# Kernel tuning notes

Hardware: AMD Instinct MI355X
Metric: run time of the kernel (lower is better)

## Reference

```python
import jax, jax.numpy as jnp
import numpy as np
from jax import lax

ANCHORS = jnp.array([[-83.0, -39.0, 100.0, 56.0], [-175.0, -87.0, 192.0, 104.0],
                     [-359.0, -183.0, 376.0, 200.0], [-55.0, -55.0, 72.0, 72.0],
                     [-119.0, -119.0, 136.0, 136.0], [-247.0, -247.0, 264.0, 264.0],
                     [-35.0, -79.0, 52.0, 96.0], [-79.0, -167.0, 96.0, 184.0],
                     [-167.0, -343.0, 184.0, 360.0]], dtype=jnp.float32)
FEAT_STRIDE = 16
NMS_THRESH = 0.7
NA = 9
PRE_NMS_TOPN = 3000   # test_pre_nms_topN
POST_NMS_TOPN = 300   # test_post_nms_topN


def setup_inputs() -> dict:
    key = jax.random.key(0)
    ks = jax.random.split(key, 4)
    B, C, H, W = 8, 512, 64, 64
    x = jax.random.normal(ks[0], (B, C, H, W), jnp.float32)
    im_size = jnp.full((B, 2), 1024.0, jnp.float32)  # (H, W) per image
    W_conv = jax.random.normal(ks[1], (512, C, 3, 3), jnp.float32) * 0.01
    b_conv = jnp.zeros((512,), jnp.float32)
    W_reg = jax.random.normal(ks[2], (36, 512), jnp.float32) * 0.01
    b_reg = jnp.zeros((36,), jnp.float32)
    W_cls = jax.random.normal(ks[3], (18, 512), jnp.float32) * 0.01
    b_cls = jnp.zeros((18,), jnp.float32)
    return {"x": x, "im_size": im_size, "W_conv": W_conv, "b_conv": b_conv,
            "W_reg": W_reg, "b_reg": b_reg, "W_cls": W_cls, "b_cls": b_cls}


def _nms_select(boxes):
    """Greedy NMS on boxes already sorted by descending score.
    Returns [POST_NMS_TOPN, 4], zero-padded (matches torch output init)."""
    M = boxes.shape[0]
    area = (boxes[:, 2] - boxes[:, 0]) * (boxes[:, 3] - boxes[:, 1])
    lt = jnp.maximum(boxes[:, None, :2], boxes[None, :, :2])
    rb = jnp.minimum(boxes[:, None, 2:], boxes[None, :, 2:])
    wh = jnp.maximum(rb - lt, 0.0)
    inter = wh[..., 0] * wh[..., 1]
    iou = inter / (area[:, None] + area[None, :] - inter + 1e-9)
    iou = lax.stop_gradient(iou)
    idxs = jnp.arange(M)

    def body(keep, i):
        sup = (iou[i] > NMS_THRESH) & (idxs > i) & keep[i]
        return keep & ~sup, None

    keep, _ = lax.scan(body, jnp.ones((M,), bool), idxs)
    key = jnp.where(keep, idxs, M)           # push suppressed to the end
    order = jnp.sort(key)[:POST_NMS_TOPN]
    valid = order < M
    gi = jnp.minimum(order, M - 1)
    return jnp.where(valid[:, None], boxes[gi], 0.0)


def reference(x, im_size, W_conv, b_conv, W_reg, b_reg, W_cls, b_cls):
    B = x.shape[0]
    conv = lax.conv_general_dilated(
        x, W_conv, window_strides=(1, 1), padding='SAME',
        dimension_numbers=('NCHW', 'OIHW', 'NCHW')) + b_conv[None, :, None, None]
    Hc, Wc = conv.shape[2], conv.shape[3]

    # bbox deltas from raw (pre-ReLU) conv features, as in the source
    reg = jnp.einsum('bchw,oc->bohw', conv, W_reg) + b_reg[None, :, None, None]
    delta = reg.transpose(0, 2, 3, 1).reshape(B, -1, 4)  # (B, H*W*9, 4)

    # scores from ReLU'd features; channel-pair softmax trick, take class 0
    feat = jax.nn.relu(conv)
    cls = jnp.einsum('bchw,oc->bohw', feat, W_cls) + b_cls[None, :, None, None]
    c2 = cls.reshape(B, 2, NA * Hc, Wc)
    scores = jax.nn.softmax(c2, axis=1)[:, 0].reshape(B, -1)  # (B, 9*H*W)

    # anchor shifting: (h, w, anchor) ordering matches delta layout
    sx = jnp.arange(Wc, dtype=x.dtype) * FEAT_STRIDE
    sy = jnp.arange(Hc, dtype=x.dtype) * FEAT_STRIDE
    gx, gy = jnp.meshgrid(sx, sy)  # (Hc, Wc) 'xy' indexing
    shifts = jnp.stack([gx.ravel(), gy.ravel(), gx.ravel(), gy.ravel()], axis=1)
    anc = (shifts[:, None, :] + ANCHORS[None, :, :]).reshape(-1, 4)  # (H*W*9, 4)

    # decode, faithful to the source's (nonstandard) math
    w = anc[:, 2] - anc[:, 0] + 1.0
    h = anc[:, 3] - anc[:, 1] + 1.0
    cx = anc[:, 0] + 0.5 * w
    cy = anc[:, 1] + 0.5 * h
    dx, dy, dw, dh = delta[..., 0], delta[..., 1], delta[..., 2], delta[..., 3]
    pcx = dx * cx
    pcy = dy * cy
    pw = jnp.exp(dw) * w
    ph = jnp.exp(dh) * h
    x1, y1 = pcx - 0.5 * pw, pcy - 0.5 * ph
    x2, y2 = pcx + 0.5 * pw, pcy + 0.5 * ph

    # clip to image bounds (im_size[i] = (H, W))
    xmax = im_size[:, 1:2] - 1.0  # (B,1)
    ymax = im_size[:, 0:1] - 1.0
    x1 = jnp.clip(x1, 0.0, xmax)
    y1 = jnp.clip(y1, 0.0, ymax)
    x2 = jnp.clip(x2, 0.0, xmax)
    y2 = jnp.clip(y2, 0.0, ymax)
    proposals = jnp.stack([x1, y1, x2, y2], axis=-1)  # (B, N, 4)

    # pre-NMS top-k by score, then greedy NMS, keep post_nms_topN
    _, top_i = lax.top_k(scores, PRE_NMS_TOPN)
    top_b = jnp.take_along_axis(proposals, top_i[..., None], axis=1)
    output = jax.vmap(_nms_select)(top_b)  # (B, POST_NMS_TOPN, 4)

    return output, scores, proposals
```

## Files before the change

### kernel.cpp

```cpp
#include <hip/hip_runtime.h>
#include <stdint.h>

typedef unsigned long long u64;
typedef double v4d __attribute__((ext_vector_type(4)));

#define NIMG 8
#define CIN 512
#define COUT 512
#define NPOS 4096
#define NSC 36864
#define PRE_TOPN 3000
#define POST_TOPN 300
#define NWORDS 47
#define MSTRIDE 48
#define WROW 66
#define WCH_DBL 2376
#define WBUF_BYTES 19008

__constant__ double dANC[9][4] = {
    {-83.0, -39.0, 100.0, 56.0},   {-175.0, -87.0, 192.0, 104.0},
    {-359.0, -183.0, 376.0, 200.0},{-55.0, -55.0, 72.0, 72.0},
    {-119.0, -119.0, 136.0, 136.0},{-247.0, -247.0, 264.0, 264.0},
    {-35.0, -79.0, 52.0, 96.0},    {-79.0, -167.0, 96.0, 184.0},
    {-167.0, -343.0, 184.0, 360.0}};

static __device__ __forceinline__ void gload16(const void* g, void* l) {
    __builtin_amdgcn_global_load_lds(
        (const __attribute__((address_space(1))) void*)g,
        (__attribute__((address_space(3))) void*)l, 16, 0, 0);
}

__global__ __launch_bounds__(256) void transpose_wconv_f64(const float* __restrict__ W,
                                                           double* __restrict__ Wtd2) {
    __shared__ float t[32][33];
    int k0 = blockIdx.x * 32;
    int o0 = blockIdx.y * 32;
    int tid = threadIdx.x;
    for (int idx = tid; idx < 1024; idx += 256) {
        int r = idx >> 5, c = idx & 31;
        t[r][c] = W[(size_t)(o0 + r) * 4608 + k0 + c];
    }
    __syncthreads();
    for (int idx = tid; idx < 1024; idx += 256) {
        int r = idx >> 5, c = idx & 31;
        int oc = o0 + c;
        Wtd2[((size_t)(oc >> 6) * 4608 + (k0 + r)) * WROW + (oc & 63)] = (double)t[c][r];
    }
}

__global__ __launch_bounds__(256) void build_wheads(const float* __restrict__ Wreg,
                                                    const float* __restrict__ Wcls,
                                                    float* __restrict__ Wh) {
    int g = blockIdx.x * 256 + threadIdx.x;
    if (g >= 512 * 64) return;
    int k = g >> 6, o = g & 63;
    float v = 0.f;
    if (o < 36) v = Wreg[o * 512 + k];
    else if (o < 54) v = Wcls[(o - 36) * 512 + k];
    Wh[g] = v;
}

__global__ __launch_bounds__(64) void mfma_probe(int* __restrict__ variant) {
    __shared__ double AA[72][16];
    __shared__ double BB[72][16];
    const int L = threadIdx.x;
    for (int i = L; i < 72 * 16; i += 64) {
        int K = i >> 4, c = i & 15;
        AA[K][c] = (double)(c * 73 + K + 1);
        BB[K][c] = (double)(K * 17 + 3 * c + 1);
    }
    __syncthreads();
    const int lg = L >> 4, lm = L & 15;
    v4d accN = {0.0, 0.0, 0.0, 0.0};
    v4d accS = {0.0, 0.0, 0.0, 0.0};
#pragma unroll
    for (int k4 = 0; k4 < 18; ++k4) {
        double a = AA[4 * k4 + lg][lm];
        double b = BB[4 * k4 + lg][lm];
        accN = __builtin_amdgcn_mfma_f64_16x16x4f64(a, b, accN, 0, 0, 0);
        accS = __builtin_amdgcn_mfma_f64_16x16x4f64(b, a, accS, 0, 0, 0);
    }
    int found = 255;
    for (int v = 0; v < 8; ++v) {
        bool ok = true;
        for (int r = 0; r < 4; ++r) {
            int m, n;
            int dm = v & 3;
            if (dm == 0)      { m = 4 * lg + r; n = lm; }
            else if (dm == 1) { m = lm; n = 4 * lg + r; }
            else if (dm == 2) { m = lg + 4 * r; n = lm; }
            else              { m = lm; n = lg + 4 * r; }
            long long ref = 0;
            for (int K = 0; K < 72; ++K)
                ref += (long long)(m * 73 + K + 1) * (long long)(K * 17 + 3 * n + 1);
            double got = (v < 4) ? accN[r] : accS[r];
            ok = ok && (got == (double)ref);
        }
        if (__all(ok) && found == 255) found = v;
    }
    if (L == 0) *variant = found;
}

__global__ __launch_bounds__(512) void conv_mfma(const float* __restrict__ X,
                                                 const double* __restrict__ Wtd2,
                                                 const float* __restrict__ bconv,
                                                 double* __restrict__ convb,
                                                 const int* __restrict__ variant,
                                                 int img_base) {
    const int vr = *variant;
    if (vr > 7) return;
    const int tid = threadIdx.x;
    const int wv = tid >> 6;
    const int lane = tid & 63;
    const int lg = lane >> 4;
    const int lm = lane & 15;
    const int ocg = wv >> 1;
    const int posb = (wv & 1) * 32;
    const int octile = blockIdx.x;
    const int oc0 = octile * 64;
    const int y = blockIdx.y;
    const int imgL = blockIdx.z;
    const int img_g = img_base + imgL;

    __shared__ double Wl[2][36][WROW];
    __shared__ float Xl[2][4][3][68];
    char* wl0 = (char*)&Wl[0][0][0];
    float* xl0 = &Xl[0][0][0][0];

    v4d acc[2];
    acc[0] = (v4d){0.0, 0.0, 0.0, 0.0};
    acc[1] = (v4d){0.0, 0.0, 0.0, 0.0};

    int boff[9];
#pragma unroll
    for (int k4 = 0; k4 < 9; ++k4) {
        int row = k4 * 4 + lg;
        int c = row / 9;
        int t = row - 9 * c;
        int ty = t / 3;
        int tx = t - 3 * ty;
        boff[k4] = (c * 3 + ty) * 68 + tx + posb + lm;
    }

    int xli1, xoff0, xoff1;
    {
        int idx = tid;
        int c_l = idx / 204;
        int rem = idx - c_l * 204;
        int r = rem / 68;
        int xx = rem - r * 68;
        int yy = y + r - 1;
        int xg = xx - 1;
        xoff0 = -1;
        if (xx < 66 && (unsigned)yy < 64u && (unsigned)xg < 64u)
            xoff0 = ((img_g * CIN + c_l) * 64 + yy) * 64 + xg;
    }
    {
        int idx = 512 + tid;
        xli1 = (idx < 816) ? idx : -1;
        xoff1 = -1;
        if (idx < 816) {
            int c_l = idx / 204;
            int rem = idx - c_l * 204;
            int r = rem / 68;
            int xx = rem - r * 68;
            int yy = y + r - 1;
            int xg = xx - 1;
            if (xx < 66 && (unsigned)yy < 64u && (unsigned)xg < 64u)
                xoff1 = ((img_g * CIN + c_l) * 64 + yy) * 64 + xg;
        }
    }
    int woff[2];
#pragma unroll
    for (int i = 0; i < 2; ++i) {
        int u = i * 512 + tid;
        int row = u / 33, cp = u - 33 * row;
        woff[i] = (octile * 4608 + row) * WROW + cp * 2;
    }
    int woff4;
    {
        int u = 1024 + tid;
        int row = u / 33, cp = u - 33 * row;
        woff4 = (octile * 4608 + row) * WROW + cp * 2;
    }

    float xr0, xr1;
    double2 wrr;

#define WDMA(c, par) { \
    gload16(&Wtd2[(size_t)woff[0] + (size_t)(c) * WCH_DBL], \
            wl0 + (size_t)(par) * WBUF_BYTES + (size_t)tid * 16); \
    gload16(&Wtd2[(size_t)woff[1] + (size_t)(c) * WCH_DBL], \
            wl0 + (size_t)(par) * WBUF_BYTES + (size_t)(512 + tid) * 16); }

#define LOADR(c) { \
    if (tid < 164) wrr = *(const double2*)&Wtd2[(size_t)woff4 + (size_t)(c) * WCH_DBL]; \
    xr0 = (xoff0 >= 0) ? X[(size_t)xoff0 + (size_t)(c) * 16384] : 0.f; \
    xr1 = (xoff1 >= 0) ? X[(size_t)xoff1 + (size_t)(c) * 16384] : 0.f; }

#define WRITER(par) { \
    if (tid < 164) \
        *(double2*)(wl0 + (size_t)(par) * WBUF_BYTES + (size_t)(1024 + tid) * 16) = wrr; \
    xl0[(size_t)(par) * 816 + tid] = xr0; \
    if (xli1 >= 0) xl0[(size_t)(par) * 816 + xli1] = xr1; }

    WDMA(0, 0);
    LOADR(0);
    WRITER(0);
    __syncthreads();

    const bool swapped = (vr >= 4);
    const int aoff = ocg * 16 + lm;

    for (int c = 0; c < 128; ++c) {
        const int par = c & 1;
        if (c < 127) { WDMA(c + 1, par ^ 1); LOADR(c + 1); }
        const double* wb = &Wl[par][0][0];
        const float* bx = xl0 + (size_t)par * 816;
        if (!swapped) {
#pragma unroll
            for (int k4 = 0; k4 < 9; ++k4) {
                double a = wb[(4 * k4 + lg) * WROW + aoff];
                const float* bp = bx + boff[k4];
                double b0 = (double)bp[0];
                double b1 = (double)bp[16];
                acc[0] = __builtin_amdgcn_mfma_f64_16x16x4f64(a, b0, acc[0], 0, 0, 0);
                acc[1] = __builtin_amdgcn_mfma_f64_16x16x4f64(a, b1, acc[1], 0, 0, 0);
            }
        } else {
#pragma unroll
            for (int k4 = 0; k4 < 9; ++k4) {
                double a = wb[(4 * k4 + lg) * WROW + aoff];
                const float* bp = bx + boff[k4];
                double b0 = (double)bp[0];
                double b1 = (double)bp[16];
                acc[0] = __builtin_amdgcn_mfma_f64_16x16x4f64(b0, a, acc[0], 0, 0, 0);
                acc[1] = __builtin_amdgcn_mfma_f64_16x16x4f64(b1, a, acc[1], 0, 0, 0);
            }
        }
        if (c < 127) { WRITER(par ^ 1); }
        __syncthreads();
    }
#undef WDMA
#undef LOADR
#undef WRITER

    const int dm = vr & 3;
#pragma unroll
    for (int q = 0; q < 2; ++q) {
#pragma unroll
        for (int r = 0; r < 4; ++r) {
            int m, n;
            if (dm == 0)      { m = 4 * lg + r; n = lm; }
            else if (dm == 1) { m = lm; n = 4 * lg + r; }
            else if (dm == 2) { m = lg + 4 * r; n = lm; }
            else              { m = lm; n = lg + 4 * r; }
            int oc = oc0 + ocg * 16 + m;
            int xp = posb + q * 16 + n;
            convb[((size_t)imgL * COUT + oc) * NPOS + y * 64 + xp] =
                acc[q][r] + (double)bconv[oc];
        }
    }
}

__global__ __launch_bounds__(256) void conv_valu(const float* __restrict__ X,
                                                 const double* __restrict__ Wtd2,
                                                 const float* __restrict__ bconv,
                                                 double* __restrict__ convb,
                                                 const int* __restrict__ variant,
                                                 int img_base) {
    if (*variant <= 7) return;
    const int tid = threadIdx.x;
    const int octile = blockIdx.x;
    const int oc0 = octile * 64;
    const int y = blockIdx.y;
    const int imgL = blockIdx.z;
    const int img_g = img_base + imgL;
    const int x_l = (tid & 15) * 4;
    const int oc_l = (tid >> 4) * 4;

    __shared__ double Wl[72][64];
    __shared__ double Bx[8][3][68];

    double acc[4][4];
#pragma unroll
    for (int i = 0; i < 4; ++i)
#pragma unroll
        for (int j = 0; j < 4; ++j) acc[i][j] = 0.0;

    for (int cc = 0; cc < CIN; cc += 8) {
        __syncthreads();
        for (int idx = tid; idx < 8 * 3 * 68; idx += 256) {
            int c_l = idx / 204;
            int rem = idx - c_l * 204;
            int r = rem / 68;
            int xx = rem - r * 68;
            int yy = y + r - 1;
            int xg = xx - 1;
            float v = 0.f;
            if (xx < 66 && (unsigned)yy < 64u && (unsigned)xg < 64u)
                v = X[(((size_t)img_g * CIN + cc + c_l) * 64 + yy) * 64 + xg];
            Bx[c_l][r][xx] = (double)v;
        }
        for (int idx = tid; idx < 72 * 32; idx += 256) {
            int kl = idx >> 5, cp = idx & 31;
            double2 v = *(const double2*)&Wtd2[((size_t)octile * 4608 + cc * 9 + kl) * WROW + cp * 2];
            *(double2*)&Wl[kl][cp * 2] = v;
        }
        __syncthreads();
#pragma unroll 2
        for (int c_l = 0; c_l < 8; ++c_l) {
#pragma unroll
            for (int ty = 0; ty < 3; ++ty) {
                double xv[6];
                *(double2*)&xv[0] = *(const double2*)&Bx[c_l][ty][x_l + 0];
                *(double2*)&xv[2] = *(const double2*)&Bx[c_l][ty][x_l + 2];
                *(double2*)&xv[4] = *(const double2*)&Bx[c_l][ty][x_l + 4];
#pragma unroll
                for (int tx = 0; tx < 3; ++tx) {
                    const double* wp = &Wl[c_l * 9 + ty * 3 + tx][oc_l];
                    double wr[4];
                    *(double2*)&wr[0] = *(const double2*)(wp + 0);
                    *(double2*)&wr[2] = *(const double2*)(wp + 2);
#pragma unroll
                    for (int i = 0; i < 4; ++i)
#pragma unroll
                        for (int j = 0; j < 4; ++j)
                            acc[i][j] = fma(wr[i], xv[j + tx], acc[i][j]);
                }
            }
        }
    }
#pragma unroll
    for (int i = 0; i < 4; ++i) {
        int oc = oc0 + oc_l + i;
        double b = (double)bconv[oc];
        double4 st;
        st.x = acc[i][0] + b; st.y = acc[i][1] + b;
        st.z = acc[i][2] + b; st.w = acc[i][3] + b;
        *(double4*)&convb[((size_t)imgL * COUT + oc) * NPOS + y * 64 + x_l] = st;
    }
}

__global__ __launch_bounds__(256) void heads_kernel(const double* __restrict__ convb,
                                                    const float* __restrict__ Wh,
                                                    const float* __restrict__ breg,
                                                    const float* __restrict__ bcls,
                                                    const float* __restrict__ im_size,
                                                    float* __restrict__ out_scores,
                                                    float4* __restrict__ out_props,
                                                    double* __restrict__ dscores,
                                                    double4* __restrict__ dprops,
                                                    int img_base) {
    const int tid = threadIdx.x;
    const int y = blockIdx.x;
    const int imgL = blockIdx.y;
    const int img_g = img_base + imgL;

    __shared__ double cl[64][64];
    __shared__ float wl[64][64];

    const int o = tid & 63;
    const int g = tid >> 6;
    double acc[16];
#pragma unroll
    for (int j = 0; j < 16; ++j) acc[j] = 0.0;

    for (int k0 = 0; k0 < CIN; k0 += 64) {
        __syncthreads();
        for (int idx = tid; idx < 4096; idx += 256) {
            int kl = idx >> 6, p = idx & 63;
            cl[kl][p] = convb[((size_t)imgL * COUT + k0 + kl) * NPOS + y * 64 + p];
        }
        for (int idx = tid; idx < 4096; idx += 256) {
            wl[idx >> 6][idx & 63] = Wh[(k0 + (idx >> 6)) * 64 + (idx & 63)];
        }
        __syncthreads();
        const bool ru = (o >= 36);
        for (int kl = 0; kl < 64; ++kl) {
            double w = (double)wl[kl][o];
#pragma unroll
            for (int j = 0; j < 16; ++j) {
                double v = cl[kl][g * 16 + j];
                if (ru) v = fmax(v, 0.0);
                acc[j] = fma(w, v, acc[j]);
            }
        }
    }
    __syncthreads();
    double bias = (o < 36) ? (double)breg[o] : (o < 54 ? (double)bcls[o - 36] : 0.0);
#pragma unroll
    for (int j = 0; j < 16; ++j) cl[o][g * 16 + j] = acc[j] + bias;
    __syncthreads();

    const double im_h = (double)im_size[img_g * 2 + 0];
    const double im_w = (double)im_size[img_g * 2 + 1];
    const double xmax = im_w - 1.0, ymax = im_h - 1.0;

    for (int t = tid; t < 576; t += 256) {
        int p = t / 9;
        int a = t - p * 9;
        double dx = cl[a * 4 + 0][p], dy = cl[a * 4 + 1][p];
        double dw = cl[a * 4 + 2][p], dh = cl[a * 4 + 3][p];
        double c0 = cl[36 + a][p], c1 = cl[45 + a][p];
        double mm = fmax(c0, c1);
        double e0 = exp(c0 - mm), e1 = exp(c1 - mm);
        double sc = e0 / (e0 + e1);

        double sx = (double)p * 16.0, sy = (double)y * 16.0;
        double a0 = dANC[a][0] + sx, a1 = dANC[a][1] + sy;
        double a2 = dANC[a][2] + sx, a3 = dANC[a][3] + sy;
        double w_ = a2 - a0 + 1.0, h_ = a3 - a1 + 1.0;
        double cx = a0 + 0.5 * w_, cy = a1 + 0.5 * h_;
        double pcx = dx * cx, pcy = dy * cy;
        double pw = exp(dw) * w_, ph = exp(dh) * h_;
        double x1 = pcx - 0.5 * pw, y1 = pcy - 0.5 * ph;
        double x2 = pcx + 0.5 * pw, y2 = pcy + 0.5 * ph;
        x1 = fmin(fmax(x1, 0.0), xmax);
        y1 = fmin(fmax(y1, 0.0), ymax);
        x2 = fmin(fmax(x2, 0.0), xmax);
        y2 = fmin(fmax(y2, 0.0), ymax);

        int pp = y * 64 + p;
        size_t si = (size_t)img_g * NSC + (size_t)a * NPOS + pp;
        size_t pi = (size_t)img_g * NSC + (size_t)pp * 9 + a;
        out_scores[si] = (float)sc;
        dscores[si] = sc;
        double4 db; db.x = x1; db.y = y1; db.z = x2; db.w = y2;
        dprops[pi] = db;
        out_props[pi] = make_float4((float)x1, (float)y1, (float)x2, (float)y2);
    }
}

__global__ __launch_bounds__(256) void topk_select(const double* __restrict__ dscores,
                                                   u64* __restrict__ Tsel) {
    const int img = blockIdx.x;
    const int tid = threadIdx.x;
    const u64* sb = (const u64*)(dscores + (size_t)img * NSC);
    __shared__ uint32_t hist[256];
    __shared__ u64 s_prefix;
    __shared__ uint32_t s_rem;
    if (tid == 0) { s_prefix = 0ull; s_rem = PRE_TOPN; }
    for (int pass = 0; pass < 8; ++pass) {
        int shift = 56 - pass * 8;
        hist[tid] = 0;
        __syncthreads();
        u64 pmask = pass ? (~0ull << (shift + 8)) : 0ull;
        u64 pref = s_prefix;
        for (int i = tid; i < NSC; i += 256) {
            u64 v = sb[i];
            if ((v & pmask) == pref) atomicAdd(&hist[(uint32_t)(v >> shift) & 0xFFu], 1u);
        }
        __syncthreads();
        if (tid == 0) {
            uint32_t rem = s_rem, cum = 0;
            int b = 255;
            for (; b > 0; --b) {
                if (cum + hist[b] >= rem) break;
                cum += hist[b];
            }
            s_prefix = pref | ((u64)(uint32_t)b << shift);
            s_rem = rem - cum;
        }
        __syncthreads();
    }
    if (tid == 0) Tsel[img] = s_prefix;
}

__global__ __launch_bounds__(1024) void sort_gather(const double* __restrict__ dscores,
                                                    const double4* __restrict__ dprops,
                                                    const u64* __restrict__ Tsel,
                                                    double4* __restrict__ dboxes) {
    const int img = blockIdx.x;
    const int tid = threadIdx.x;
    __shared__ u64 skey[4096];
    __shared__ unsigned short sidx[4096];
    __shared__ int cnt;
    if (tid == 0) cnt = 0;
    for (int i = tid; i < 4096; i += 1024) { skey[i] = 0ull; sidx[i] = 0xFFFF; }
    __syncthreads();
    const u64 T = Tsel[img];
    const u64* sb = (const u64*)(dscores + (size_t)img * NSC);
    for (int i = tid; i < NSC; i += 1024) {
        u64 v = sb[i];
        if (v >= T) {
            int p = atomicAdd(&cnt, 1);
            if (p < 4096) { skey[p] = v; sidx[p] = (unsigned short)i; }
        }
    }
    __syncthreads();
    for (int k = 2; k <= 4096; k <<= 1) {
        for (int j = k >> 1; j > 0; j >>= 1) {
            for (int i = tid; i < 4096; i += 1024) {
                int ixj = i ^ j;
                if (ixj > i) {
                    u64 ka = skey[i], kb = skey[ixj];
                    unsigned short ia = sidx[i], ib = sidx[ixj];
                    bool aw = (ka < kb) || (ka == kb && ia > ib);
                    bool up = (i & k) == 0;
                    if (up ? aw : !aw) {
                        skey[i] = kb; skey[ixj] = ka;
                        sidx[i] = ib; sidx[ixj] = ia;
                    }
                }
            }
            __syncthreads();
        }
    }
    for (int t = tid; t < PRE_TOPN; t += 1024) {
        unsigned int idx = sidx[t];
        dboxes[(size_t)img * PRE_TOPN + t] = dprops[(size_t)img * NSC + idx];
    }
}

__global__ __launch_bounds__(256) void iou_mask_kernel(const double4* __restrict__ dboxes,
                                                       u64* __restrict__ mask) {
    const int tid = threadIdx.x;
    const int ib = blockIdx.x;
    const int img = blockIdx.y;
    const int i = ib * 64 + (tid >> 2);
    if (i >= PRE_TOPN) return;
    const double4 bi = dboxes[(size_t)img * PRE_TOPN + i];
    const double ai = (bi.z - bi.x) * (bi.w - bi.y);
    for (int w = (tid & 3); w < NWORDS; w += 4) {
        const int jbase = w * 64;
        u64 m = 0;
        if (jbase + 63 > i) {
            const int jmax = min(64, PRE_TOPN - jbase);
            for (int b = 0; b < jmax; ++b) {
                int j = jbase + b;
                if (j > i) {
                    double4 bj = dboxes[(size_t)img * PRE_TOPN + j];
                    double aj = (bj.z - bj.x) * (bj.w - bj.y);
                    double ltx = fmax(bi.x, bj.x), lty = fmax(bi.y, bj.y);
                    double rbx = fmin(bi.z, bj.z), rby = fmin(bi.w, bj.w);
                    double iw = fmax(rbx - ltx, 0.0), ih = fmax(rby - lty, 0.0);
                    double inter = iw * ih;
                    double iou = inter / (ai + aj - inter + 1e-9);
                    if (iou > 0.7) m |= (1ull << b);
                }
            }
        }
        mask[((size_t)img * PRE_TOPN + i) * MSTRIDE + w] = m;
    }
}

__global__ __launch_bounds__(64) void nms_walk(const double4* __restrict__ dboxes,
                                               const u64* __restrict__ mask,
                                               float4* __restrict__ outb) {
    const int img = blockIdx.x;
    const int lane = threadIdx.x;
    __shared__ u64 removed[NWORDS];
    __shared__ short kept[POST_TOPN];
    __shared__ int nk;
    if (lane < NWORDS) removed[lane] = 0ull;
    if (lane == 0) nk = 0;
    __syncthreads();
    for (int i = 0; i < PRE_TOPN; ++i) {
        u64 rw = removed[i >> 6];
        int cur = nk;
        if (!((rw >> (i & 63)) & 1ull)) {
            if (lane == 0) { kept[cur] = (short)i; nk = cur + 1; }
            if (cur + 1 >= POST_TOPN) break;
            if (lane < NWORDS)
                removed[lane] |= mask[((size_t)img * PRE_TOPN + i) * MSTRIDE + lane];
        }
        __syncthreads();
    }
    __syncthreads();
    const int n = nk;
    for (int r = lane; r < POST_TOPN; r += 64) {
        float4 v = make_float4(0.f, 0.f, 0.f, 0.f);
        if (r < n) {
            double4 d = dboxes[(size_t)img * PRE_TOPN + kept[r]];
            v = make_float4((float)d.x, (float)d.y, (float)d.z, (float)d.w);
        }
        outb[img * POST_TOPN + r] = v;
    }
}

extern "C" void kernel_launch(void* const* d_in, const int* in_sizes, int n_in,
                              void* d_out, int out_size, void* d_ws, size_t ws_size,
                              hipStream_t stream) {
    const float* x = (const float*)d_in[0];
    const float* im_size = (const float*)d_in[1];
    const float* Wconv = (const float*)d_in[2];
    const float* bconv = (const float*)d_in[3];
    const float* Wreg = (const float*)d_in[4];
    const float* breg = (const float*)d_in[5];
    const float* Wcls = (const float*)d_in[6];
    const float* bcls = (const float*)d_in[7];

    float* outf = (float*)d_out;
    float4* out_boxes = (float4*)outf;
    float* out_scores = outf + NIMG * POST_TOPN * 4;
    float4* out_props = (float4*)(out_scores + (size_t)NIMG * NSC);

    char* ws = (char*)d_ws;
    const size_t WT_OFF = 0;
    const size_t WH_OFF = WT_OFF + (size_t)8 * 4608 * WROW * 8;
    const size_t TS_OFF = WH_OFF + (size_t)512 * 64 * 4;
    const size_t VAR_OFF = TS_OFF + 64;
    const size_t DS_OFF = (VAR_OFF + 4 + 255) & ~(size_t)255;
    const size_t DP_OFF = DS_OFF + (size_t)NIMG * NSC * 8;
    const size_t DB_OFF = DP_OFF + (size_t)NIMG * NSC * 32;
    const size_t MK_OFF = DB_OFF + (size_t)NIMG * PRE_TOPN * 32;
    const size_t CV_OFF = (MK_OFF + (size_t)NIMG * PRE_TOPN * MSTRIDE * 8 + 255) & ~(size_t)255;

    double* Wtd2 = (double*)(ws + WT_OFF);
    float* Wh = (float*)(ws + WH_OFF);
    u64* Tsel = (u64*)(ws + TS_OFF);
    int* variant = (int*)(ws + VAR_OFF);
    double* dscores = (double*)(ws + DS_OFF);
    double4* dprops = (double4*)(ws + DP_OFF);
    double4* dboxes = (double4*)(ws + DB_OFF);
    u64* mask = (u64*)(ws + MK_OFF);
    double* convb = (double*)(ws + CV_OFF);

    const size_t per_img = (size_t)COUT * NPOS * 8;
    int CH = 1;
    if (ws_size > CV_OFF + per_img) {
        size_t avail = (ws_size - CV_OFF) / per_img;
        CH = (int)(avail > 8 ? 8 : avail);
        if (CH < 1) CH = 1;
    }

    transpose_wconv_f64<<<dim3(144, 16), 256, 0, stream>>>(Wconv, Wtd2);
    build_wheads<<<128, 256, 0, stream>>>(Wreg, Wcls, Wh);
    mfma_probe<<<1, 64, 0, stream>>>(variant);

    for (int base = 0; base < NIMG; base += CH) {
        int n = NIMG - base;
        if (n > CH) n = CH;
        conv_mfma<<<dim3(8, 64, n), 512, 0, stream>>>(x, Wtd2, bconv, convb, variant, base);
        conv_valu<<<dim3(8, 64, n), 256, 0, stream>>>(x, Wtd2, bconv, convb, variant, base);
        heads_kernel<<<dim3(64, n), 256, 0, stream>>>(convb, Wh, breg, bcls, im_size,
                                                      out_scores, out_props,
                                                      dscores, dprops, base);
    }
    topk_select<<<NIMG, 256, 0, stream>>>(dscores, Tsel);
    sort_gather<<<NIMG, 1024, 0, stream>>>(dscores, dprops, Tsel, dboxes);
    iou_mask_kernel<<<dim3(NWORDS, NIMG), 256, 0, stream>>>(dboxes, mask);
    nms_walk<<<NIMG, 64, 0, stream>>>(dboxes, mask, out_boxes);
}
```

Measured before the change: 3.616 ms.

## Process two output rows per conv block with 2x2 MFMA register tile per wave

Each conv_mfma block now covers two output rows instead of one, halving the grid along y. The input halo grows from three to four rows so the weight tile is reused across both rows, and each wave computes a 2x2 grid of 16x16 MFMA tiles (two output-channel groups by two position groups). This roughly halves global and LDS weight traffic per output and raises MFMA work per LDS read, at the cost of more accumulator registers and fewer blocks in flight.

```diff
diff --git a/kernel.cpp b/kernel.cpp
--- a/kernel.cpp
+++ b/kernel.cpp
@@ -16,6 +16,7 @@
 #define WROW 66
 #define WCH_DBL 2376
 #define WBUF_BYTES 19008
+#define XBUF 1088
 
 __constant__ double dANC[9][4] = {
     {-83.0, -39.0, 100.0, 56.0},   {-175.0, -87.0, 192.0, 104.0},
@@ -114,22 +115,25 @@
     const int lane = tid & 63;
     const int lg = lane >> 4;
     const int lm = lane & 15;
-    const int ocg = wv >> 1;
-    const int posb = (wv & 1) * 32;
+    const int ocg = wv & 1;
+    const int yh = (wv >> 1) & 1;
+    const int ph = wv >> 2;
     const int octile = blockIdx.x;
     const int oc0 = octile * 64;
-    const int y = blockIdx.y;
+    const int y0 = blockIdx.y * 2;
     const int imgL = blockIdx.z;
     const int img_g = img_base + imgL;
 
     __shared__ double Wl[2][36][WROW];
-    __shared__ float Xl[2][4][3][68];
+    __shared__ float Xl[2][4][4][68];
     char* wl0 = (char*)&Wl[0][0][0];
     float* xl0 = &Xl[0][0][0][0];
 
-    v4d acc[2];
-    acc[0] = (v4d){0.0, 0.0, 0.0, 0.0};
-    acc[1] = (v4d){0.0, 0.0, 0.0, 0.0};
+    v4d acc[2][2];
+#pragma unroll
+    for (int oq = 0; oq < 2; ++oq)
+#pragma unroll
+        for (int pq = 0; pq < 2; ++pq) acc[oq][pq] = (v4d){0.0, 0.0, 0.0, 0.0};
 
     int boff[9];
 #pragma unroll
@@ -139,36 +143,43 @@
         int t = row - 9 * c;
         int ty = t / 3;
         int tx = t - 3 * ty;
-        boff[k4] = (c * 3 + ty) * 68 + tx + posb + lm;
-    }
-
-    int xli1, xoff0, xoff1;
+        boff[k4] = (c * 4 + yh + ty) * 68 + tx + ph * 32 + lm;
+    }
+
+    int xoff0, xoff1, xoff2;
     {
         int idx = tid;
-        int c_l = idx / 204;
-        int rem = idx - c_l * 204;
+        int c_l = idx / 272;
+        int rem = idx - c_l * 272;
         int r = rem / 68;
         int xx = rem - r * 68;
-        int yy = y + r - 1;
+        int yy = y0 + r - 1;
         int xg = xx - 1;
-        xoff0 = -1;
-        if (xx < 66 && (unsigned)yy < 64u && (unsigned)xg < 64u)
-            xoff0 = ((img_g * CIN + c_l) * 64 + yy) * 64 + xg;
+        xoff0 = (xx < 66 && (unsigned)yy < 64u && (unsigned)xg < 64u)
+                    ? ((img_g * CIN + c_l) * 64 + yy) * 64 + xg : -1;
     }
     {
         int idx = 512 + tid;
-        xli1 = (idx < 816) ? idx : -1;
-        xoff1 = -1;
-        if (idx < 816) {
-            int c_l = idx / 204;
-            int rem = idx - c_l * 204;
-            int r = rem / 68;
-            int xx = rem - r * 68;
-            int yy = y + r - 1;
-            int xg = xx - 1;
-            if (xx < 66 && (unsigned)yy < 64u && (unsigned)xg < 64u)
-                xoff1 = ((img_g * CIN + c_l) * 64 + yy) * 64 + xg;
-        }
+        int c_l = idx / 272;
+        int rem = idx - c_l * 272;
+        int r = rem / 68;
+        int xx = rem - r * 68;
+        int yy = y0 + r - 1;
+        int xg = xx - 1;
+        xoff1 = (xx < 66 && (unsigned)yy < 64u && (unsigned)xg < 64u)
+                    ? ((img_g * CIN + c_l) * 64 + yy) * 64 + xg : -1;
+    }
+    xoff2 = -1;
+    if (tid < 64) {
+        int idx = 1024 + tid;
+        int c_l = idx / 272;
+        int rem = idx - c_l * 272;
+        int r = rem / 68;
+        int xx = rem - r * 68;
+        int yy = y0 + r - 1;
+        int xg = xx - 1;
+        if (xx < 66 && (unsigned)yy < 64u && (unsigned)xg < 64u)
+            xoff2 = ((img_g * CIN + c_l) * 64 + yy) * 64 + xg;
     }
     int woff[2];
 #pragma unroll
@@ -184,7 +195,7 @@
         woff4 = (octile * 4608 + row) * WROW + cp * 2;
     }
 
-    float xr0, xr1;
+    float xr0, xr1, xr2;
     double2 wrr;
 
 #define WDMA(c, par) { \
@@ -196,13 +207,15 @@
 #define LOADR(c) { \
     if (tid < 164) wrr = *(const double2*)&Wtd2[(size_t)woff4 + (size_t)(c) * WCH_DBL]; \
     xr0 = (xoff0 >= 0) ? X[(size_t)xoff0 + (size_t)(c) * 16384] : 0.f; \
-    xr1 = (xoff1 >= 0) ? X[(size_t)xoff1 + (size_t)(c) * 16384] : 0.f; }
+    xr1 = (xoff1 >= 0) ? X[(size_t)xoff1 + (size_t)(c) * 16384] : 0.f; \
+    xr2 = (xoff2 >= 0) ? X[(size_t)xoff2 + (size_t)(c) * 16384] : 0.f; }
 
 #define WRITER(par) { \
     if (tid < 164) \
         *(double2*)(wl0 + (size_t)(par) * WBUF_BYTES + (size_t)(1024 + tid) * 16) = wrr; \
-    xl0[(size_t)(par) * 816 + tid] = xr0; \
-    if (xli1 >= 0) xl0[(size_t)(par) * 816 + xli1] = xr1; }
+    xl0[(size_t)(par) * XBUF + tid] = xr0; \
+    xl0[(size_t)(par) * XBUF + 512 + tid] = xr1; \
+    if (tid < 64) xl0[(size_t)(par) * XBUF + 1024 + tid] = xr2; }
 
     WDMA(0, 0);
     LOADR(0);
@@ -210,32 +223,40 @@
     __syncthreads();
 
     const bool swapped = (vr >= 4);
-    const int aoff = ocg * 16 + lm;
+    const int aoff0 = ocg * 32 + lm;
 
     for (int c = 0; c < 128; ++c) {
         const int par = c & 1;
         if (c < 127) { WDMA(c + 1, par ^ 1); LOADR(c + 1); }
         const double* wb = &Wl[par][0][0];
-        const float* bx = xl0 + (size_t)par * 816;
+        const float* bx = xl0 + (size_t)par * XBUF;
         if (!swapped) {
 #pragma unroll
             for (int k4 = 0; k4 < 9; ++k4) {
-                double a = wb[(4 * k4 + lg) * WROW + aoff];
+                const double* wp = wb + (4 * k4 + lg) * WROW + aoff0;
+                double a0 = wp[0];
+                double a1 = wp[16];
                 const float* bp = bx + boff[k4];
                 double b0 = (double)bp[0];
                 double b1 = (double)bp[16];
-                acc[0] = __builtin_amdgcn_mfma_f64_16x16x4f64(a, b0, acc[0], 0, 0, 0);
-                acc[1] = __builtin_amdgcn_mfma_f64_16x16x4f64(a, b1, acc[1], 0, 0, 0);
+                acc[0][0] = __builtin_amdgcn_mfma_f64_16x16x4f64(a0, b0, acc[0][0], 0, 0, 0);
+                acc[0][1] = __builtin_amdgcn_mfma_f64_16x16x4f64(a0, b1, acc[0][1], 0, 0, 0);
+                acc[1][0] = __builtin_amdgcn_mfma_f64_16x16x4f64(a1, b0, acc[1][0], 0, 0, 0);
+                acc[1][1] = __builtin_amdgcn_mfma_f64_16x16x4f64(a1, b1, acc[1][1], 0, 0, 0);
             }
         } else {
 #pragma unroll
             for (int k4 = 0; k4 < 9; ++k4) {
-                double a = wb[(4 * k4 + lg) * WROW + aoff];
+                const double* wp = wb + (4 * k4 + lg) * WROW + aoff0;
+                double a0 = wp[0];
+                double a1 = wp[16];
                 const float* bp = bx + boff[k4];
                 double b0 = (double)bp[0];
                 double b1 = (double)bp[16];
-                acc[0] = __builtin_amdgcn_mfma_f64_16x16x4f64(b0, a, acc[0], 0, 0, 0);
-                acc[1] = __builtin_amdgcn_mfma_f64_16x16x4f64(b1, a, acc[1], 0, 0, 0);
+                acc[0][0] = __builtin_amdgcn_mfma_f64_16x16x4f64(b0, a0, acc[0][0], 0, 0, 0);
+                acc[0][1] = __builtin_amdgcn_mfma_f64_16x16x4f64(b1, a0, acc[0][1], 0, 0, 0);
+                acc[1][0] = __builtin_amdgcn_mfma_f64_16x16x4f64(b0, a1, acc[1][0], 0, 0, 0);
+                acc[1][1] = __builtin_amdgcn_mfma_f64_16x16x4f64(b1, a1, acc[1][1], 0, 0, 0);
             }
         }
         if (c < 127) { WRITER(par ^ 1); }
@@ -246,19 +267,23 @@
 #undef WRITER
 
     const int dm = vr & 3;
-#pragma unroll
-    for (int q = 0; q < 2; ++q) {
-#pragma unroll
-        for (int r = 0; r < 4; ++r) {
-            int m, n;
-            if (dm == 0)      { m = 4 * lg + r; n = lm; }
-            else if (dm == 1) { m = lm; n = 4 * lg + r; }
-            else if (dm == 2) { m = lg + 4 * r; n = lm; }
-            else              { m = lm; n = lg + 4 * r; }
-            int oc = oc0 + ocg * 16 + m;
-            int xp = posb + q * 16 + n;
-            convb[((size_t)imgL * COUT + oc) * NPOS + y * 64 + xp] =
-                acc[q][r] + (double)bconv[oc];
+    const int yrow = y0 + yh;
+#pragma unroll
+    for (int oq = 0; oq < 2; ++oq) {
+#pragma unroll
+        for (int pq = 0; pq < 2; ++pq) {
+#pragma unroll
+            for (int r = 0; r < 4; ++r) {
+                int m, n;
+                if (dm == 0)      { m = 4 * lg + r; n = lm; }
+                else if (dm == 1) { m = lm; n = 4 * lg + r; }
+                else if (dm == 2) { m = lg + 4 * r; n = lm; }
+                else              { m = lm; n = lg + 4 * r; }
+                int oc = oc0 + ocg * 32 + oq * 16 + m;
+                int xp = ph * 32 + pq * 16 + n;
+                convb[((size_t)imgL * COUT + oc) * NPOS + yrow * 64 + xp] =
+                    acc[oq][pq][r] + (double)bconv[oc];
+            }
         }
     }
 }
@@ -632,7 +657,7 @@
     for (int base = 0; base < NIMG; base += CH) {
         int n = NIMG - base;
         if (n > CH) n = CH;
-        conv_mfma<<<dim3(8, 64, n), 512, 0, stream>>>(x, Wtd2, bconv, convb, variant, base);
+        conv_mfma<<<dim3(8, 32, n), 512, 0, stream>>>(x, Wtd2, bconv, convb, variant, base);
         conv_valu<<<dim3(8, 64, n), 256, 0, stream>>>(x, Wtd2, bconv, convb, variant, base);
         heads_kernel<<<dim3(64, n), 256, 0, stream>>>(convb, Wh, breg, bcls, im_size,
                                                       out_scores, out_props,
```

Result: slower. 3.778 ms (+4.5%).
